# Kernel optimization log

Measured on AMD Instinct MI355X. Metric: run time of the kernel, lower is better.

## Reference

```python
import jax, jax.numpy as jnp
import numpy as np

NUM_GRAPHS = 64


def gcn_conv(x, edge_index, W, b):
    # PyG GCNConv: x' = D^-1/2 (A+I) D^-1/2 (x W) + b, self-loops added.
    n = x.shape[0]
    h = x @ W  # [N, out]
    loop = jnp.arange(n)
    src = jnp.concatenate([edge_index[0], loop])
    dst = jnp.concatenate([edge_index[1], loop])
    deg = jax.ops.segment_sum(jnp.ones_like(dst, dtype=h.dtype), dst, num_segments=n)
    dinv = jnp.where(deg > 0, jax.lax.rsqrt(deg), 0.0)
    norm = dinv[src] * dinv[dst]  # [E+N]
    msgs = h[src] * norm[:, None]  # gather + scale
    out = jax.ops.segment_sum(msgs, dst, num_segments=n)  # scatter-add
    return out + b


def lstm_step(x, W_ih, W_hh, b_ih, b_hh):
    # single time step, zero initial state; PyTorch gate order i,f,g,o
    H = W_hh.shape[1]
    gates = x @ W_ih.T + b_ih + b_hh  # h0 = 0 so W_hh term vanishes
    i, f, g, o = jnp.split(gates, 4, axis=-1)
    i, f, o = jax.nn.sigmoid(i), jax.nn.sigmoid(f), jax.nn.sigmoid(o)
    c = i * jnp.tanh(g)  # f * c0 = 0
    return o * jnp.tanh(c)


def setup_inputs() -> dict:
    key = jax.random.key(0)
    ks = jax.random.split(key, 16)
    N, E, F, G, H, C = 50000, 600000, 128, 128, 256, 1
    s = lambda *sh: 1.0 / np.sqrt(sh[-1])
    return {
        "x": jax.random.normal(ks[0], (N, F), jnp.float32),
        "edge_index": jax.random.randint(ks[1], (2, E), 0, N),
        "batch": jnp.sort(jax.random.randint(ks[2], (N,), 0, NUM_GRAPHS)),
        "W1": jax.random.normal(ks[3], (F, G), jnp.float32) * s(F, G),
        "b1": jnp.zeros((G,), jnp.float32),
        "W2": jax.random.normal(ks[4], (G, G), jnp.float32) * s(G, G),
        "b2": jnp.zeros((G,), jnp.float32),
        "W_ih": jax.random.normal(ks[5], (4 * H, G), jnp.float32) * s(4 * H, G),
        "W_hh": jax.random.normal(ks[6], (4 * H, H), jnp.float32) * s(4 * H, H),
        "b_ih": jnp.zeros((4 * H,), jnp.float32),
        "b_hh": jnp.zeros((4 * H,), jnp.float32),
        "Wm": jax.random.normal(ks[7], (C, H), jnp.float32) * s(C, H),
        "bm": jnp.zeros((C,), jnp.float32),
        "Wv": jax.random.normal(ks[8], (C, H), jnp.float32) * s(C, H),
        "bv": jnp.zeros((C,), jnp.float32),
    }


def reference(x, edge_index, batch, W1, b1, W2, b2, W_ih, W_hh, b_ih, b_hh, Wm, bm, Wv, bv):
    h = jax.nn.relu(gcn_conv(x, edge_index, W1, b1))
    h = jax.nn.relu(gcn_conv(h, edge_index, W2, b2))
    # global mean pool over graphs
    sums = jax.ops.segment_sum(h, batch, num_segments=NUM_GRAPHS)
    cnts = jax.ops.segment_sum(jnp.ones_like(batch, dtype=h.dtype), batch, num_segments=NUM_GRAPHS)
    pooled = sums / jnp.maximum(cnts, 1.0)[:, None]  # [G_graphs, gcn_hidden]
    hT = lstm_step(pooled, W_ih, W_hh, b_ih, b_hh)  # [G_graphs, lstm_hidden]
    mean = hT @ Wm.T + bm
    log_var = jax.nn.softplus(hT @ Wv.T + bv)
    return (mean, log_var)
```

## Files before the change

### kernel.cpp

```cpp
#include <hip/hip_runtime.h>
#include <hip/hip_bf16.h>
#include <math.h>


#define POOL_SUB 32

typedef __attribute__((ext_vector_type(8))) short bf16x8;
typedef __attribute__((ext_vector_type(4))) float f32x4;

static __device__ __forceinline__ unsigned short f2bf(float f) {
    union { float f; unsigned int u; } v; v.f = f;
    unsigned int u = v.u;
    unsigned int r = u + 0x7FFFu + ((u >> 16) & 1u);
    return (unsigned short)(r >> 16);
}
static __device__ __forceinline__ unsigned int pack2bf(float lo, float hi) {
    return (unsigned int)f2bf(lo) | ((unsigned int)f2bf(hi) << 16);
}
static __device__ __forceinline__ float bflo(unsigned int v) {
    union { unsigned int u; float f; } w; w.u = v << 16; return w.f;
}
static __device__ __forceinline__ float bfhi(unsigned int v) {
    union { unsigned int u; float f; } w; w.u = v & 0xFFFF0000u; return w.f;
}
static __device__ __forceinline__ bf16x8 f8_to_bf(float4 f0, float4 f1) {
    union { unsigned int u[4]; bf16x8 v; } r;
    r.u[0] = pack2bf(f0.x, f0.y);
    r.u[1] = pack2bf(f0.z, f0.w);
    r.u[2] = pack2bf(f1.x, f1.y);
    r.u[3] = pack2bf(f1.z, f1.w);
    return r.v;
}

__global__ __launch_bounds__(256) void prep_kernel(int* __restrict__ zp, int zwords,
                                                   const float* __restrict__ W1,
                                                   const float* __restrict__ W2,
                                                   unsigned short* __restrict__ Wt1,
                                                   unsigned short* __restrict__ Wt2, int zb) {
    int b = blockIdx.x;
    int t = threadIdx.x;
    if (b < zb) {
        int i = b * 256 + t;
        if (i < zwords) zp[i] = 0;
    } else {
        int col = b - zb;
        if (t < 128) Wt1[col * 128 + t] = f2bf(W1[(size_t)t * 128 + col]);
        else { int k = t - 128; Wt2[col * 128 + k] = f2bf(W2[(size_t)k * 128 + col]); }
    }
}

__global__ void count_deg_kernel(const int* __restrict__ dst, int E, int* __restrict__ deg) {
    int e = blockIdx.x * blockDim.x + threadIdx.x;
    if (e < E) atomicAdd(&deg[dst[e]], 1);
}

__global__ void scan_pass1(const int* __restrict__ deg, int n,
                           int* __restrict__ rowptr, int* __restrict__ bsums) {
    __shared__ int s[256];
    int tid = threadIdx.x;
    int base = blockIdx.x * 1024;
    int v[4];
    int mysum = 0;
#pragma unroll
    for (int j = 0; j < 4; ++j) {
        int idx = base + tid * 4 + j;
        v[j] = (idx < n) ? deg[idx] : 0;
        mysum += v[j];
    }
    s[tid] = mysum;
    __syncthreads();
    for (int off = 1; off < 256; off <<= 1) {
        int t = (tid >= off) ? s[tid - off] : 0;
        __syncthreads();
        s[tid] += t;
        __syncthreads();
    }
    int excl = s[tid] - mysum;
#pragma unroll
    for (int j = 0; j < 4; ++j) {
        int idx = base + tid * 4 + j;
        if (idx < n) rowptr[idx] = excl;
        excl += v[j];
    }
    if (tid == 255) bsums[blockIdx.x] = s[255];
}

__global__ void scan_pass23(int* __restrict__ rowptr, const int* __restrict__ bsums,
                            const int* __restrict__ deg, float* __restrict__ dinv,
                            int n, int nb) {
    __shared__ int sm[64];
    __shared__ int pref[65];
    int tid = threadIdx.x;
    if (tid < 64) sm[tid] = (tid < nb) ? bsums[tid] : 0;
    __syncthreads();
    if (tid == 0) {
        int s = 0;
#pragma unroll 8
        for (int i = 0; i < 64; ++i) { pref[i] = s; s += sm[i]; }
        pref[64] = s;
    }
    __syncthreads();
    int add = pref[blockIdx.x];
    int base = blockIdx.x * 1024;
#pragma unroll
    for (int j = 0; j < 4; ++j) {
        int idx = base + tid * 4 + j;
        if (idx < n) {
            rowptr[idx] += add;
            dinv[idx] = rsqrtf((float)deg[idx] + 1.0f);
        }
    }
    if (blockIdx.x == 0 && tid == 0) rowptr[n] = pref[64];
}

__global__ void fill_csr_kernel(const int* __restrict__ src, const int* __restrict__ dst, int E,
                                const int* __restrict__ rowptr, int* __restrict__ cursor,
                                int* __restrict__ csr) {
    int e = blockIdx.x * blockDim.x + threadIdx.x;
    if (e < E) {
        int d = dst[e];
        int pos = rowptr[d] + atomicAdd(&cursor[d], 1);
        csr[pos] = src[e];
    }
}

__global__ __launch_bounds__(256) void gemm_mfma_f32a_kernel(const float* __restrict__ A,
                                                             const unsigned short* __restrict__ Wt,
                                                             const float* __restrict__ dinv,
                                                             unsigned short* __restrict__ out,
                                                             int n) {
    int tid = threadIdx.x;
    int l = tid & 63;
    int wid = tid >> 6;
    int rowbase = blockIdx.x * 64 + wid * 16;
    int lc = l & 15;
    int kq = l >> 4;

    int arow = rowbase + lc; if (arow > n - 1) arow = n - 1;
    const float* Ap = A + (size_t)arow * 128 + kq * 8;
    const unsigned short* Wp = Wt + (size_t)lc * 128 + kq * 8;

    f32x4 acc[8];
#pragma unroll
    for (int c = 0; c < 8; ++c) acc[c] = (f32x4){0.f, 0.f, 0.f, 0.f};

#pragma unroll
    for (int ks = 0; ks < 4; ++ks) {
        float4 f0 = *(const float4*)(Ap + ks * 32);
        float4 f1 = *(const float4*)(Ap + ks * 32 + 4);
        bf16x8 a = f8_to_bf(f0, f1);
#pragma unroll
        for (int c = 0; c < 8; ++c) {
            bf16x8 b = *(const bf16x8*)(Wp + c * 2048 + ks * 32);
            acc[c] = __builtin_amdgcn_mfma_f32_16x16x32_bf16(a, b, acc[c], 0, 0, 0);
        }
    }

    int r0 = kq * 4;
    float s[4];
    int orow[4];
#pragma unroll
    for (int r = 0; r < 4; ++r) {
        orow[r] = rowbase + r0 + r;
        s[r] = (orow[r] < n) ? dinv[orow[r]] : 0.f;
    }
#pragma unroll
    for (int c = 0; c < 8; ++c) {
#pragma unroll
        for (int r = 0; r < 4; ++r) {
            if (orow[r] < n)
                out[(size_t)orow[r] * 128 + c * 16 + lc] = f2bf(acc[c][r] * s[r]);
        }
    }
}

__global__ __launch_bounds__(256) void gemm_mfma_kernel(const unsigned short* __restrict__ A,
                                                        const unsigned short* __restrict__ Wt,
                                                        const float* __restrict__ dinv,
                                                        unsigned short* __restrict__ out,
                                                        int n) {
    int tid = threadIdx.x;
    int l = tid & 63;
    int wid = tid >> 6;
    int rowbase = blockIdx.x * 64 + wid * 16;
    int lc = l & 15;
    int kq = l >> 4;

    int arow = rowbase + lc; if (arow > n - 1) arow = n - 1;
    const unsigned short* Ap = A + (size_t)arow * 128 + kq * 8;
    const unsigned short* Wp = Wt + (size_t)lc * 128 + kq * 8;

    f32x4 acc[8];
#pragma unroll
    for (int c = 0; c < 8; ++c) acc[c] = (f32x4){0.f, 0.f, 0.f, 0.f};

#pragma unroll
    for (int ks = 0; ks < 4; ++ks) {
        bf16x8 a = *(const bf16x8*)(Ap + ks * 32);
#pragma unroll
        for (int c = 0; c < 8; ++c) {
            bf16x8 b = *(const bf16x8*)(Wp + c * 2048 + ks * 32);
            acc[c] = __builtin_amdgcn_mfma_f32_16x16x32_bf16(a, b, acc[c], 0, 0, 0);
        }
    }

    int r0 = kq * 4;
    float s[4];
    int orow[4];
#pragma unroll
    for (int r = 0; r < 4; ++r) {
        orow[r] = rowbase + r0 + r;
        s[r] = (orow[r] < n) ? dinv[orow[r]] : 0.f;
    }
#pragma unroll
    for (int c = 0; c < 8; ++c) {
#pragma unroll
        for (int r = 0; r < 4; ++r) {
            if (orow[r] < n)
                out[(size_t)orow[r] * 128 + c * 16 + lc] = f2bf(acc[c][r] * s[r]);
        }
    }
}

__global__ __launch_bounds__(256) void aggregate_kernel(const uint2* __restrict__ g2,
                                                        const int* __restrict__ rowptr,
                                                        const int* __restrict__ csr,
                                                        const float* __restrict__ dinv,
                                                        const float* __restrict__ bias,
                                                        uint2* __restrict__ out, int n) {
    int lane = threadIdx.x & 63;
    int node = (blockIdx.x * blockDim.x + threadIdx.x) >> 6;
    if (node >= n) return;
    int li = lane & 31, pair = lane >> 5;
    int beg = rowptr[node], end = rowptr[node + 1];
    float a0 = 0.f, a1 = 0.f, a2 = 0.f, a3 = 0.f;
    int e = beg;
    for (; e + 4 <= end; e += 4) {
        uint2 v = g2[(size_t)csr[e + pair] * 32 + li];
        uint2 w = g2[(size_t)csr[e + 2 + pair] * 32 + li];
        a0 += bflo(v.x) + bflo(w.x); a1 += bfhi(v.x) + bfhi(w.x);
        a2 += bflo(v.y) + bflo(w.y); a3 += bfhi(v.y) + bfhi(w.y);
    }
    if (e + 2 <= end) {
        uint2 v = g2[(size_t)csr[e + pair] * 32 + li];
        a0 += bflo(v.x); a1 += bfhi(v.x);
        a2 += bflo(v.y); a3 += bfhi(v.y);
        e += 2;
    }
    if (e + pair < end) {
        uint2 v = g2[(size_t)csr[e + pair] * 32 + li];
        a0 += bflo(v.x); a1 += bfhi(v.x);
        a2 += bflo(v.y); a3 += bfhi(v.y);
    }
    a0 += __shfl_xor(a0, 32, 64);
    a1 += __shfl_xor(a1, 32, 64);
    a2 += __shfl_xor(a2, 32, 64);
    a3 += __shfl_xor(a3, 32, 64);
    if (pair == 0) {
        uint2 sv = g2[(size_t)node * 32 + li];
        float dv = dinv[node];
        float4 b = ((const float4*)bias)[li];
        float r0 = fmaxf(dv * (a0 + bflo(sv.x)) + b.x, 0.f);
        float r1 = fmaxf(dv * (a1 + bfhi(sv.x)) + b.y, 0.f);
        float r2 = fmaxf(dv * (a2 + bflo(sv.y)) + b.z, 0.f);
        float r3 = fmaxf(dv * (a3 + bfhi(sv.y)) + b.w, 0.f);
        out[(size_t)node * 32 + li] = make_uint2(pack2bf(r0, r1), pack2bf(r2, r3));
    }
}

__global__ __launch_bounds__(64) void pool_partial_kernel(const unsigned int* __restrict__ h,
                                                          const int* __restrict__ batch, int n,
                                                          float* __restrict__ partial) {
    int g = blockIdx.x / POOL_SUB;
    int sub = blockIdx.x % POOL_SUB;
    int t = threadIdx.x;
    int lo = 0, hi = n;
    while (lo < hi) { int mid = (lo + hi) >> 1; if (batch[mid] < g) lo = mid + 1; else hi = mid; }
    int start = lo;
    hi = n;
    while (lo < hi) { int mid = (lo + hi) >> 1; if (batch[mid] < g + 1) lo = mid + 1; else hi = mid; }
    int end = lo;
    int len = end - start;
    int b0 = start + (int)((long long)len * sub / POOL_SUB);
    int b1 = start + (int)((long long)len * (sub + 1) / POOL_SUB);
    float ax = 0.f, ay = 0.f;
    int i = b0;
    for (; i + 4 <= b1; i += 4) {
        unsigned int v0 = h[(size_t)(i + 0) * 64 + t];
        unsigned int v1 = h[(size_t)(i + 1) * 64 + t];
        unsigned int v2 = h[(size_t)(i + 2) * 64 + t];
        unsigned int v3 = h[(size_t)(i + 3) * 64 + t];
        ax += bflo(v0) + bflo(v1) + bflo(v2) + bflo(v3);
        ay += bfhi(v0) + bfhi(v1) + bfhi(v2) + bfhi(v3);
    }
    for (; i < b1; ++i) {
        unsigned int v0 = h[(size_t)i * 64 + t];
        ax += bflo(v0);
        ay += bfhi(v0);
    }
    partial[(size_t)blockIdx.x * 128 + 2 * t]     = ax;
    partial[(size_t)blockIdx.x * 128 + 2 * t + 1] = ay;
}

__global__ __launch_bounds__(256) void pool_lstm_kernel(const float* __restrict__ partial,
                                                        const int* __restrict__ batch, int n,
                                                        const float* __restrict__ W_ih,
                                                        const float* __restrict__ b_ih,
                                                        const float* __restrict__ b_hh,
                                                        const float* __restrict__ Wm,
                                                        const float* __restrict__ bm,
                                                        const float* __restrict__ Wv,
                                                        const float* __restrict__ bv,
                                                        float* __restrict__ out) {
    __shared__ __align__(16) float p[128];
    __shared__ float redm[256];
    __shared__ float redv[256];
    int gph = blockIdx.x;
    int tid = threadIdx.x;
    if (tid < 128) {
        int lo = 0, hi = n;
        while (lo < hi) { int mid = (lo + hi) >> 1; if (batch[mid] < gph) lo = mid + 1; else hi = mid; }
        int start = lo;
        hi = n;
        while (lo < hi) { int mid = (lo + hi) >> 1; if (batch[mid] < gph + 1) lo = mid + 1; else hi = mid; }
        int end = lo;
        float acc = 0.f;
#pragma unroll
        for (int s = 0; s < POOL_SUB; ++s)
            acc += partial[(size_t)(gph * POOL_SUB + s) * 128 + tid];
        p[tid] = acc / fmaxf((float)(end - start), 1.0f);
    }
    __syncthreads();
    float gi = b_ih[tid] + b_hh[tid];
    float gg = b_ih[512 + tid] + b_hh[512 + tid];
    float go = b_ih[768 + tid] + b_hh[768 + tid];
    const float4* wi = (const float4*)(W_ih + (size_t)tid * 128);
    const float4* wg = (const float4*)(W_ih + (size_t)(512 + tid) * 128);
    const float4* wo = (const float4*)(W_ih + (size_t)(768 + tid) * 128);
    const float4* p4 = (const float4*)p;
#pragma unroll 8
    for (int k = 0; k < 32; ++k) {
        float4 xv = p4[k];
        float4 a = wi[k], bq = wg[k], cq = wo[k];
        gi += xv.x * a.x + xv.y * a.y + xv.z * a.z + xv.w * a.w;
        gg += xv.x * bq.x + xv.y * bq.y + xv.z * bq.z + xv.w * bq.w;
        go += xv.x * cq.x + xv.y * cq.y + xv.z * cq.z + xv.w * cq.w;
    }
    float iv = 1.f / (1.f + expf(-gi));
    float cv = iv * tanhf(gg);
    float ov = 1.f / (1.f + expf(-go));
    float hT = ov * tanhf(cv);
    redm[tid] = hT * Wm[tid];
    redv[tid] = hT * Wv[tid];
    __syncthreads();
    for (int s = 128; s > 0; s >>= 1) {
        if (tid < s) { redm[tid] += redm[tid + s]; redv[tid] += redv[tid + s]; }
        __syncthreads();
    }
    if (tid == 0) {
        out[gph] = redm[0] + bm[0];
        float xv = redv[0] + bv[0];
        out[64 + gph] = fmaxf(xv, 0.f) + log1pf(expf(-fabsf(xv)));
    }
}

extern "C" void kernel_launch(void* const* d_in, const int* in_sizes, int n_in,
                              void* d_out, int out_size, void* d_ws, size_t ws_size,
                              hipStream_t stream) {
    const float* x     = (const float*)d_in[0];
    const int*   edge  = (const int*)d_in[1];
    const int*   batch = (const int*)d_in[2];
    const float* W1    = (const float*)d_in[3];
    const float* b1    = (const float*)d_in[4];
    const float* W2    = (const float*)d_in[5];
    const float* b2    = (const float*)d_in[6];
    const float* W_ih  = (const float*)d_in[7];
    const float* b_ih  = (const float*)d_in[9];
    const float* b_hh  = (const float*)d_in[10];
    const float* Wm    = (const float*)d_in[11];
    const float* bm    = (const float*)d_in[12];
    const float* Wv    = (const float*)d_in[13];
    const float* bv    = (const float*)d_in[14];
    float* out = (float*)d_out;

    const int N = in_sizes[0] / 128;
    const int E = in_sizes[1] / 2;
    const int* srcIdx = edge;
    const int* dstIdx = edge + E;

    char* ws = (char*)d_ws;
    size_t off = 0;
    const size_t gB = (size_t)N * 64 * sizeof(unsigned int);
    unsigned int* gbuf = (unsigned int*)(ws + off); off += gB;
    unsigned int* hbuf = (unsigned int*)(ws + off); off += gB;
    int* deg    = (int*)(ws + off);   off += (size_t)N * sizeof(int);
    int* cursor = (int*)(ws + off);   off += (size_t)N * sizeof(int);
    int* rowptr = (int*)(ws + off);   off += (size_t)(N + 1) * sizeof(int);
    off = (off + 255) & ~(size_t)255;
    int* bsums  = (int*)(ws + off);   off += 512;
    int* csr    = (int*)(ws + off);   off += (size_t)E * sizeof(int);
    off = (off + 255) & ~(size_t)255;
    float* dinv = (float*)(ws + off); off += (size_t)N * sizeof(float);
    off = (off + 255) & ~(size_t)255;
    unsigned short* Wt1 = (unsigned short*)(ws + off); off += 128 * 128 * sizeof(unsigned short);
    unsigned short* Wt2 = (unsigned short*)(ws + off); off += 128 * 128 * sizeof(unsigned short);
    off = (off + 255) & ~(size_t)255;
    float* partial = (float*)(ws + off); off += (size_t)64 * POOL_SUB * 128 * sizeof(float);

    int zwords = 2 * N;
    int zb = (zwords + 255) / 256;
    prep_kernel<<<zb + 128, 256, 0, stream>>>(deg, zwords, W1, W2, Wt1, Wt2, zb);

    int eb = (E + 255) / 256;
    count_deg_kernel<<<eb, 256, 0, stream>>>(dstIdx, E, deg);

    int nb = (N + 1023) / 1024;
    scan_pass1<<<nb, 256, 0, stream>>>(deg, N, rowptr, bsums);
    scan_pass23<<<nb, 256, 0, stream>>>(rowptr, bsums, deg, dinv, N, nb);
    fill_csr_kernel<<<eb, 256, 0, stream>>>(srcIdx, dstIdx, E, rowptr, cursor, csr);

    int gb = (N + 63) / 64;
    int ab = (N + 3) / 4;

    gemm_mfma_f32a_kernel<<<gb, 256, 0, stream>>>(x, Wt1, dinv, (unsigned short*)gbuf, N);
    aggregate_kernel<<<ab, 256, 0, stream>>>((const uint2*)gbuf, rowptr, csr, dinv, b1, (uint2*)hbuf, N);
    gemm_mfma_kernel<<<gb, 256, 0, stream>>>((const unsigned short*)hbuf, Wt2, dinv, (unsigned short*)gbuf, N);
    aggregate_kernel<<<ab, 256, 0, stream>>>((const uint2*)gbuf, rowptr, csr, dinv, b2, (uint2*)hbuf, N);

    pool_partial_kernel<<<64 * POOL_SUB, 64, 0, stream>>>(hbuf, batch, N, partial);
    pool_lstm_kernel<<<64, 256, 0, stream>>>(partial, batch, N, W_ih, b_ih, b_hh, Wm, bm, Wv, bv, out);
}
```

Before: 227.9 us.

## Store GEMM outputs as FP8 for aggregation gathers and merge scan into one kernel

The GEMM epilogues now write the dinv-scaled node features as FP8 instead of bf16 when the conversion builtins exist. This halves the bytes gathered per edge in the aggregation kernels, which now use a 16-lane by 4-edge layout with packed FP8-to-f32 conversions. Separately, the two-pass degree scan becomes one single-block kernel that loops over chunks, removing a launch and the block-sum buffer but running serially on one block. FP8 storage adds quantization error to intermediate features, which may exceed tolerance.

After: 283.3 us. 1.24x slower.

```diff
diff --git a/kernel.cpp b/kernel.cpp
--- a/kernel.cpp
+++ b/kernel.cpp
@@ -5,8 +5,15 @@
 
 #define POOL_SUB 32
 
+#if __has_builtin(__builtin_amdgcn_cvt_pk_f32_fp8) && __has_builtin(__builtin_amdgcn_cvt_pk_fp8_f32)
+#define USE_FP8 1
+#else
+#define USE_FP8 0
+#endif
+
 typedef __attribute__((ext_vector_type(8))) short bf16x8;
 typedef __attribute__((ext_vector_type(4))) float f32x4;
+typedef __attribute__((ext_vector_type(2))) float f32x2;
 
 static __device__ __forceinline__ unsigned short f2bf(float f) {
     union { float f; unsigned int u; } v; v.f = f;
@@ -31,6 +38,11 @@
     r.u[3] = pack2bf(f1.z, f1.w);
     return r.v;
 }
+#if USE_FP8
+static __device__ __forceinline__ unsigned char f2fp8(float f) {
+    return (unsigned char)(__builtin_amdgcn_cvt_pk_fp8_f32(f, f, 0, false) & 0xFF);
+}
+#endif
 
 __global__ __launch_bounds__(256) void prep_kernel(int* __restrict__ zp, int zwords,
                                                    const float* __restrict__ W1,
@@ -54,63 +66,46 @@
     if (e < E) atomicAdd(&deg[dst[e]], 1);
 }
 
-__global__ void scan_pass1(const int* __restrict__ deg, int n,
-                           int* __restrict__ rowptr, int* __restrict__ bsums) {
+__global__ __launch_bounds__(256) void scan_all_kernel(const int* __restrict__ deg,
+                                                       int* __restrict__ rowptr,
+                                                       float* __restrict__ dinv,
+                                                       int n, int nchunks) {
     __shared__ int s[256];
     int tid = threadIdx.x;
-    int base = blockIdx.x * 1024;
-    int v[4];
-    int mysum = 0;
-#pragma unroll
-    for (int j = 0; j < 4; ++j) {
-        int idx = base + tid * 4 + j;
-        v[j] = (idx < n) ? deg[idx] : 0;
-        mysum += v[j];
-    }
-    s[tid] = mysum;
-    __syncthreads();
-    for (int off = 1; off < 256; off <<= 1) {
-        int t = (tid >= off) ? s[tid - off] : 0;
+    int running = 0;
+    for (int c = 0; c < nchunks; ++c) {
+        int base = c * 1024;
+        int v[4];
+        int mysum = 0;
+#pragma unroll
+        for (int j = 0; j < 4; ++j) {
+            int idx = base + tid * 4 + j;
+            v[j] = (idx < n) ? deg[idx] : 0;
+            mysum += v[j];
+        }
+        s[tid] = mysum;
         __syncthreads();
-        s[tid] += t;
+        for (int off = 1; off < 256; off <<= 1) {
+            int t = (tid >= off) ? s[tid - off] : 0;
+            __syncthreads();
+            s[tid] += t;
+            __syncthreads();
+        }
+        int excl = running + s[tid] - mysum;
+        int total = s[255];
+#pragma unroll
+        for (int j = 0; j < 4; ++j) {
+            int idx = base + tid * 4 + j;
+            if (idx < n) {
+                rowptr[idx] = excl;
+                dinv[idx] = rsqrtf((float)v[j] + 1.0f);
+            }
+            excl += v[j];
+        }
+        running += total;
         __syncthreads();
     }
-    int excl = s[tid] - mysum;
-#pragma unroll
-    for (int j = 0; j < 4; ++j) {
-        int idx = base + tid * 4 + j;
-        if (idx < n) rowptr[idx] = excl;
-        excl += v[j];
-    }
-    if (tid == 255) bsums[blockIdx.x] = s[255];
-}
-
-__global__ void scan_pass23(int* __restrict__ rowptr, const int* __restrict__ bsums,
-                            const int* __restrict__ deg, float* __restrict__ dinv,
-                            int n, int nb) {
-    __shared__ int sm[64];
-    __shared__ int pref[65];
-    int tid = threadIdx.x;
-    if (tid < 64) sm[tid] = (tid < nb) ? bsums[tid] : 0;
-    __syncthreads();
-    if (tid == 0) {
-        int s = 0;
-#pragma unroll 8
-        for (int i = 0; i < 64; ++i) { pref[i] = s; s += sm[i]; }
-        pref[64] = s;
-    }
-    __syncthreads();
-    int add = pref[blockIdx.x];
-    int base = blockIdx.x * 1024;
-#pragma unroll
-    for (int j = 0; j < 4; ++j) {
-        int idx = base + tid * 4 + j;
-        if (idx < n) {
-            rowptr[idx] += add;
-            dinv[idx] = rsqrtf((float)deg[idx] + 1.0f);
-        }
-    }
-    if (blockIdx.x == 0 && tid == 0) rowptr[n] = pref[64];
+    if (tid == 0) rowptr[n] = running;
 }
 
 __global__ void fill_csr_kernel(const int* __restrict__ src, const int* __restrict__ dst, int E,
@@ -124,10 +119,17 @@
     }
 }
 
+
+#if USE_FP8
+#define G_STORE(outp, row, col, val) ((unsigned char*)(outp))[(size_t)(row) * 128 + (col)] = f2fp8(val)
+#else
+#define G_STORE(outp, row, col, val) ((unsigned short*)(outp))[(size_t)(row) * 128 + (col)] = f2bf(val)
+#endif
+
 __global__ __launch_bounds__(256) void gemm_mfma_f32a_kernel(const float* __restrict__ A,
                                                              const unsigned short* __restrict__ Wt,
                                                              const float* __restrict__ dinv,
-                                                             unsigned short* __restrict__ out,
+                                                             void* __restrict__ out,
                                                              int n) {
     int tid = threadIdx.x;
     int l = tid & 63;
@@ -168,8 +170,7 @@
     for (int c = 0; c < 8; ++c) {
 #pragma unroll
         for (int r = 0; r < 4; ++r) {
-            if (orow[r] < n)
-                out[(size_t)orow[r] * 128 + c * 16 + lc] = f2bf(acc[c][r] * s[r]);
+            if (orow[r] < n) G_STORE(out, orow[r], c * 16 + lc, acc[c][r] * s[r]);
         }
     }
 }
@@ -177,7 +178,7 @@
 __global__ __launch_bounds__(256) void gemm_mfma_kernel(const unsigned short* __restrict__ A,
                                                         const unsigned short* __restrict__ Wt,
                                                         const float* __restrict__ dinv,
-                                                        unsigned short* __restrict__ out,
+                                                        void* __restrict__ out,
                                                         int n) {
     int tid = threadIdx.x;
     int l = tid & 63;
@@ -216,18 +217,84 @@
     for (int c = 0; c < 8; ++c) {
 #pragma unroll
         for (int r = 0; r < 4; ++r) {
-            if (orow[r] < n)
-                out[(size_t)orow[r] * 128 + c * 16 + lc] = f2bf(acc[c][r] * s[r]);
-        }
-    }
-}
-
-__global__ __launch_bounds__(256) void aggregate_kernel(const uint2* __restrict__ g2,
+            if (orow[r] < n) G_STORE(out, orow[r], c * 16 + lc, acc[c][r] * s[r]);
+        }
+    }
+}
+
+#if USE_FP8
+__global__ __launch_bounds__(256) void aggregate_kernel(const void* __restrict__ gv,
                                                         const int* __restrict__ rowptr,
                                                         const int* __restrict__ csr,
                                                         const float* __restrict__ dinv,
                                                         const float* __restrict__ bias,
-                                                        uint2* __restrict__ out, int n) {
+                                                        unsigned int* __restrict__ out, int n) {
+    const uint2* __restrict__ g2 = (const uint2*)gv;
+    int lane = threadIdx.x & 63;
+    int node = (blockIdx.x * blockDim.x + threadIdx.x) >> 6;
+    if (node >= n) return;
+    int li = lane & 15, quad = lane >> 4;
+    int beg = rowptr[node], end = rowptr[node + 1];
+    float a0 = 0.f, a1 = 0.f, a2 = 0.f, a3 = 0.f;
+    float a4 = 0.f, a5 = 0.f, a6 = 0.f, a7 = 0.f;
+    int e = beg;
+    for (; e + 4 <= end; e += 4) {
+        uint2 v = g2[(size_t)csr[e + quad] * 16 + li];
+        f32x2 p0 = __builtin_amdgcn_cvt_pk_f32_fp8(v.x, false);
+        f32x2 p1 = __builtin_amdgcn_cvt_pk_f32_fp8(v.x, true);
+        f32x2 p2 = __builtin_amdgcn_cvt_pk_f32_fp8(v.y, false);
+        f32x2 p3 = __builtin_amdgcn_cvt_pk_f32_fp8(v.y, true);
+        a0 += p0.x; a1 += p0.y; a2 += p1.x; a3 += p1.y;
+        a4 += p2.x; a5 += p2.y; a6 += p3.x; a7 += p3.y;
+    }
+    if (e + quad < end) {
+        uint2 v = g2[(size_t)csr[e + quad] * 16 + li];
+        f32x2 p0 = __builtin_amdgcn_cvt_pk_f32_fp8(v.x, false);
+        f32x2 p1 = __builtin_amdgcn_cvt_pk_f32_fp8(v.x, true);
+        f32x2 p2 = __builtin_amdgcn_cvt_pk_f32_fp8(v.y, false);
+        f32x2 p3 = __builtin_amdgcn_cvt_pk_f32_fp8(v.y, true);
+        a0 += p0.x; a1 += p0.y; a2 += p1.x; a3 += p1.y;
+        a4 += p2.x; a5 += p2.y; a6 += p3.x; a7 += p3.y;
+    }
+    a0 += __shfl_xor(a0, 16, 64); a0 += __shfl_xor(a0, 32, 64);
+    a1 += __shfl_xor(a1, 16, 64); a1 += __shfl_xor(a1, 32, 64);
+    a2 += __shfl_xor(a2, 16, 64); a2 += __shfl_xor(a2, 32, 64);
+    a3 += __shfl_xor(a3, 16, 64); a3 += __shfl_xor(a3, 32, 64);
+    a4 += __shfl_xor(a4, 16, 64); a4 += __shfl_xor(a4, 32, 64);
+    a5 += __shfl_xor(a5, 16, 64); a5 += __shfl_xor(a5, 32, 64);
+    a6 += __shfl_xor(a6, 16, 64); a6 += __shfl_xor(a6, 32, 64);
+    a7 += __shfl_xor(a7, 16, 64); a7 += __shfl_xor(a7, 32, 64);
+    if (quad == 0) {
+        uint2 sv = g2[(size_t)node * 16 + li];
+        f32x2 s0 = __builtin_amdgcn_cvt_pk_f32_fp8(sv.x, false);
+        f32x2 s1 = __builtin_amdgcn_cvt_pk_f32_fp8(sv.x, true);
+        f32x2 s2 = __builtin_amdgcn_cvt_pk_f32_fp8(sv.y, false);
+        f32x2 s3 = __builtin_amdgcn_cvt_pk_f32_fp8(sv.y, true);
+        float dv = dinv[node];
+        float4 bl = ((const float4*)bias)[li * 2];
+        float4 bh = ((const float4*)bias)[li * 2 + 1];
+        float r0 = fmaxf(dv * (a0 + s0.x) + bl.x, 0.f);
+        float r1 = fmaxf(dv * (a1 + s0.y) + bl.y, 0.f);
+        float r2 = fmaxf(dv * (a2 + s1.x) + bl.z, 0.f);
+        float r3 = fmaxf(dv * (a3 + s1.y) + bl.w, 0.f);
+        float r4 = fmaxf(dv * (a4 + s2.x) + bh.x, 0.f);
+        float r5 = fmaxf(dv * (a5 + s2.y) + bh.y, 0.f);
+        float r6 = fmaxf(dv * (a6 + s3.x) + bh.z, 0.f);
+        float r7 = fmaxf(dv * (a7 + s3.y) + bh.w, 0.f);
+        uint4 o;
+        o.x = pack2bf(r0, r1); o.y = pack2bf(r2, r3);
+        o.z = pack2bf(r4, r5); o.w = pack2bf(r6, r7);
+        ((uint4*)out)[(size_t)node * 16 + li] = o;
+    }
+}
+#else
+__global__ __launch_bounds__(256) void aggregate_kernel(const void* __restrict__ gv,
+                                                        const int* __restrict__ rowptr,
+                                                        const int* __restrict__ csr,
+                                                        const float* __restrict__ dinv,
+                                                        const float* __restrict__ bias,
+                                                        unsigned int* __restrict__ out, int n) {
+    const uint2* __restrict__ g2 = (const uint2*)gv;
     int lane = threadIdx.x & 63;
     int node = (blockIdx.x * blockDim.x + threadIdx.x) >> 6;
     if (node >= n) return;
@@ -235,17 +302,10 @@
     int beg = rowptr[node], end = rowptr[node + 1];
     float a0 = 0.f, a1 = 0.f, a2 = 0.f, a3 = 0.f;
     int e = beg;
-    for (; e + 4 <= end; e += 4) {
-        uint2 v = g2[(size_t)csr[e + pair] * 32 + li];
-        uint2 w = g2[(size_t)csr[e + 2 + pair] * 32 + li];
-        a0 += bflo(v.x) + bflo(w.x); a1 += bfhi(v.x) + bfhi(w.x);
-        a2 += bflo(v.y) + bflo(w.y); a3 += bfhi(v.y) + bfhi(w.y);
-    }
-    if (e + 2 <= end) {
+    for (; e + 2 <= end; e += 2) {
         uint2 v = g2[(size_t)csr[e + pair] * 32 + li];
         a0 += bflo(v.x); a1 += bfhi(v.x);
         a2 += bflo(v.y); a3 += bfhi(v.y);
-        e += 2;
     }
     if (e + pair < end) {
         uint2 v = g2[(size_t)csr[e + pair] * 32 + li];
@@ -264,9 +324,10 @@
         float r1 = fmaxf(dv * (a1 + bfhi(sv.x)) + b.y, 0.f);
         float r2 = fmaxf(dv * (a2 + bflo(sv.y)) + b.z, 0.f);
         float r3 = fmaxf(dv * (a3 + bfhi(sv.y)) + b.w, 0.f);
-        out[(size_t)node * 32 + li] = make_uint2(pack2bf(r0, r1), pack2bf(r2, r3));
-    }
-}
+        ((uint2*)out)[(size_t)node * 32 + li] = make_uint2(pack2bf(r0, r1), pack2bf(r2, r3));
+    }
+}
+#endif
 
 __global__ __launch_bounds__(64) void pool_partial_kernel(const unsigned int* __restrict__ h,
                                                           const int* __restrict__ batch, int n,
@@ -391,13 +452,12 @@
     char* ws = (char*)d_ws;
     size_t off = 0;
     const size_t gB = (size_t)N * 64 * sizeof(unsigned int);
-    unsigned int* gbuf = (unsigned int*)(ws + off); off += gB;
+    void* gbuf = (void*)(ws + off); off += gB;
     unsigned int* hbuf = (unsigned int*)(ws + off); off += gB;
     int* deg    = (int*)(ws + off);   off += (size_t)N * sizeof(int);
     int* cursor = (int*)(ws + off);   off += (size_t)N * sizeof(int);
     int* rowptr = (int*)(ws + off);   off += (size_t)(N + 1) * sizeof(int);
     off = (off + 255) & ~(size_t)255;
-    int* bsums  = (int*)(ws + off);   off += 512;
     int* csr    = (int*)(ws + off);   off += (size_t)E * sizeof(int);
     off = (off + 255) & ~(size_t)255;
     float* dinv = (float*)(ws + off); off += (size_t)N * sizeof(float);
@@ -414,18 +474,17 @@
     int eb = (E + 255) / 256;
     count_deg_kernel<<<eb, 256, 0, stream>>>(dstIdx, E, deg);
 
-    int nb = (N + 1023) / 1024;
-    scan_pass1<<<nb, 256, 0, stream>>>(deg, N, rowptr, bsums);
-    scan_pass23<<<nb, 256, 0, stream>>>(rowptr, bsums, deg, dinv, N, nb);
+    int nchunks = (N + 1023) / 1024;
+    scan_all_kernel<<<1, 256, 0, stream>>>(deg, rowptr, dinv, N, nchunks);
     fill_csr_kernel<<<eb, 256, 0, stream>>>(srcIdx, dstIdx, E, rowptr, cursor, csr);
 
     int gb = (N + 63) / 64;
     int ab = (N + 3) / 4;
 
-    gemm_mfma_f32a_kernel<<<gb, 256, 0, stream>>>(x, Wt1, dinv, (unsigned short*)gbuf, N);
-    aggregate_kernel<<<ab, 256, 0, stream>>>((const uint2*)gbuf, rowptr, csr, dinv, b1, (uint2*)hbuf, N);
-    gemm_mfma_kernel<<<gb, 256, 0, stream>>>((const unsigned short*)hbuf, Wt2, dinv, (unsigned short*)gbuf, N);
-    aggregate_kernel<<<ab, 256, 0, stream>>>((const uint2*)gbuf, rowptr, csr, dinv, b2, (uint2*)hbuf, N);
+    gemm_mfma_f32a_kernel<<<gb, 256, 0, stream>>>(x, Wt1, dinv, gbuf, N);
+    aggregate_kernel<<<ab, 256, 0, stream>>>(gbuf, rowptr, csr, dinv, b1, hbuf, N);
+    gemm_mfma_kernel<<<gb, 256, 0, stream>>>((const unsigned short*)hbuf, Wt2, dinv, gbuf, N);
+    aggregate_kernel<<<ab, 256, 0, stream>>>(gbuf, rowptr, csr, dinv, b2, hbuf, N);
 
     pool_partial_kernel<<<64 * POOL_SUB, 64, 0, stream>>>(hbuf, batch, N, partial);
     pool_lstm_kernel<<<64, 256, 0, stream>>>(partial, batch, N, W_ih, b_ih, b_hh, Wm, bm, Wv, bv, out);
```
